# Optimization experiments

Hardware: AMD Instinct MI355X
Metric: run time of the kernel (lower is better)

The kernel has to match this reference:

```python
import jax, jax.numpy as jnp
import numpy as np

B, N, E = 16, 5000, 40000
IN_DIM, HID, GRU_OUT = 128, 512, 16
G0, G1, G2 = 1, 128, 128          # gcn_dim = [1,128,128]
M0, M1, M2 = 512, 1024, N * GRU_OUT  # gru_out_linear MLP dims (hidden_num prepended)
EPS = 1e-5                         # BatchNorm1d eps (eval: running mean 0, var 1)


def _gcn_norm(edge_index, n):
    loop = jnp.arange(n)
    src = jnp.concatenate([edge_index[0], loop])
    dst = jnp.concatenate([edge_index[1], loop])
    deg = jax.ops.segment_sum(jnp.ones(src.shape[0], jnp.float32), dst, num_segments=n)
    dinv = 1.0 / jnp.sqrt(deg)
    return src, dst, dinv[src] * dinv[dst]


def _gcn_conv(h, W, b, src, dst, norm):
    hw = jnp.einsum('bnf,fg->bng', h, W)
    msgs = hw[:, src, :] * norm[None, :, None]            # [B,E+N,Fout]
    agg = jax.ops.segment_sum(jnp.swapaxes(msgs, 0, 1), dst, num_segments=h.shape[1])
    return jnp.swapaxes(agg, 0, 1) + b


def _gru_cell(x, h, Wih, Whh, bih, bhh):
    gi = x @ Wih.T + bih
    gh = h @ Whh.T + bhh
    ir, iz, ig = jnp.split(gi, 3, axis=-1)
    hr, hz, hg = jnp.split(gh, 3, axis=-1)
    r = jax.nn.sigmoid(ir + hr)
    z = jax.nn.sigmoid(iz + hz)
    n = jnp.tanh(ig + r * hg)
    return (1.0 - z) * n + z * h


def _mlp_block(x, W, b, a, g, be):
    # Dropout(eval)=Identity -> Linear -> PReLU -> BatchNorm1d(eval, rm=0, rv=1)
    y = x @ W.T + b
    y = jnp.where(y >= 0, y, a * y)
    return y / jnp.sqrt(1.0 + EPS) * g + be


def setup_inputs():
    key = jax.random.key(0)
    ks = jax.random.split(key, 32)
    f = lambda i, shp, s=0.02: jax.random.normal(ks[i], shp, jnp.float32) * s
    return dict(
        x=jax.random.normal(ks[0], (B, IN_DIM), jnp.float32),
        smoothed_vert_pos=jax.random.normal(ks[1], (B, N * 3), jnp.float32),
        edge_index=jax.random.randint(ks[2], (2, E), 0, N),
        Wih=f(3, (3 * HID, IN_DIM)), Whh=f(4, (3 * HID, HID)),
        bih=f(5, (3 * HID,)), bhh=f(6, (3 * HID,)),
        Wg1=f(7, (G0, G1), 0.1), bg1=f(8, (G1,)),
        Wg2=f(9, (G1, G2), 0.1), bg2=f(10, (G2,)),
        W1=f(11, (M1, M0)), b1=f(12, (M1,)),
        a1=jnp.full((M1,), 0.25, jnp.float32),
        g1=1.0 + f(13, (M1,)), be1=f(14, (M1,)),
        W2=f(15, (M2, M1), 0.01), b2=f(16, (M2,)),
        a2=jnp.full((M2,), 0.25, jnp.float32),
        g2=1.0 + f(17, (M2,)), be2=f(18, (M2,)),
        Wo=f(19, (1, G2 + GRU_OUT)), bo=f(20, (1,)),
    )


def reference(x, smoothed_vert_pos, edge_index, Wih, Whh, bih, bhh,
              Wg1, bg1, Wg2, bg2, W1, b1, a1, g1, be1,
              W2, b2, a2, g2, be2, Wo, bo):
    b = x.shape[0]
    svp = smoothed_vert_pos.reshape(b, N, 3)
    src, dst, norm = _gcn_norm(edge_index, N)
    z = svp[:, :, 2:3]                                   # channel j+2, j=0
    h1 = _gcn_conv(z, Wg1, bg1, src, dst, norm)          # [B,N,G1], no nonlinearity between convs (as in source)
    res = _gcn_conv(h1, Wg2, bg2, src, dst, norm)        # [B,N,G2]
    hidden = jnp.zeros((b, HID), x.dtype)                # hidden=None path
    next_hidden = _gru_cell(x, hidden, Wih, Whh, bih, bhh)
    m = _mlp_block(next_hidden, W1, b1, a1, g1, be1)
    m = _mlp_block(m, W2, b2, a2, g2, be2)
    gru_out = m.reshape(b, N, GRU_OUT)
    y = jnp.concatenate([gru_out, res], axis=2) @ Wo.T + bo  # [B,N,1]
    return y.reshape(b, N), next_hidden
```

## Files before the change

### kernel.cpp

```cpp
#include <hip/hip_runtime.h>
#include <hip/hip_bf16.h>

#define NN 5000
#define BB 16
#define EE 40000
#define INF 128
#define HID 512
#define M1D 1024
#define EPSV 1e-5f

typedef float f4 __attribute__((ext_vector_type(4)));

__device__ __forceinline__ float dot4(f4 a, f4 b) {
    return fmaf(a.x, b.x, fmaf(a.y, b.y, fmaf(a.z, b.z, a.w * b.w)));
}
__device__ __forceinline__ f4 ntload(const float* p) {
    return __builtin_nontemporal_load((const f4*)p);
}

#define GRU_BLOCKS 128
#define DEG_BLOCKS 157
#define ZPACK_BLOCKS 313
#define ZERO_BLOCKS 157

__global__ __launch_bounds__(256)
void k_s1(const int* __restrict__ ei, const float* __restrict__ x,
          const float* __restrict__ svp,
          const float* __restrict__ Wih, const float* __restrict__ bih,
          const float* __restrict__ bhh,
          const float* __restrict__ Wg1, const float* __restrict__ bg1,
          const float* __restrict__ Wg2, const float* __restrict__ bg2,
          const float* __restrict__ Wo, const float* __restrict__ bo,
          float* __restrict__ deg, float* __restrict__ nh,
          float* __restrict__ outNH, float* __restrict__ cst,
          float* __restrict__ zpack, float* __restrict__ zerobase) {
    const int blk = blockIdx.x;
    const int tid = threadIdx.x;

    if (blk < GRU_BLOCKS) {
        const int t = blk * 256 + tid;
        const int q = t & 3, idx = t >> 2;
        const int b = idx >> 9, h = idx & 511;
        const float* xb = x + b * INF;
        const float* wr = Wih + (size_t)h * INF;
        const float* wz = Wih + (size_t)(HID + h) * INF;
        const float* wg = Wih + (size_t)(2 * HID + h) * INF;
        float ir = 0.f, iz = 0.f, ig = 0.f;
        #pragma unroll 8
        for (int i = 0; i < 8; ++i) {
            const int k0 = i * 16 + q * 4;
            const f4 xv = *(const f4*)(xb + k0);
            ir += dot4(xv, *(const f4*)(wr + k0));
            iz += dot4(xv, *(const f4*)(wz + k0));
            ig += dot4(xv, *(const f4*)(wg + k0));
        }
        ir += __shfl_xor(ir, 1); ir += __shfl_xor(ir, 2);
        iz += __shfl_xor(iz, 1); iz += __shfl_xor(iz, 2);
        ig += __shfl_xor(ig, 1); ig += __shfl_xor(ig, 2);
        if (q == 0) {
            ir += bih[h]; iz += bih[HID + h]; ig += bih[2 * HID + h];
            float r  = 1.f / (1.f + expf(-(ir + bhh[h])));
            float z  = 1.f / (1.f + expf(-(iz + bhh[HID + h])));
            float nv = tanhf(ig + r * bhh[2 * HID + h]);
            float v  = (1.f - z) * nv;
            nh[idx] = v;
            outNH[idx] = v;
        }
    } else if (blk < GRU_BLOCKS + DEG_BLOCKS) {
        const int e = (blk - GRU_BLOCKS) * 256 + tid;
        if (e < EE) atomicAdd(&deg[ei[EE + e]], 1.0f);
    } else if (blk == GRU_BLOCKS + DEG_BLOCKS) {
        __shared__ float su[128], sv[128], sc[128];
        const int g = tid;
        if (g < 128) {
            float t = 0.f;
            for (int c = 0; c < 128; ++c) t = fmaf(Wg2[g * 128 + c], Wo[16 + c], t);
            su[g] = Wg1[g] * t;
            sv[g] = bg1[g] * t;
            sc[g] = bg2[g] * Wo[16 + g];
        }
        __syncthreads();
        for (int s = 64; s > 0; s >>= 1) {
            if (g < s) { su[g] += su[g + s]; sv[g] += sv[g + s]; sc[g] += sc[g + s]; }
            __syncthreads();
        }
        if (g == 0) { cst[0] = su[0]; cst[1] = sv[0]; cst[2] = sc[0] + bo[0]; }
    } else if (blk < GRU_BLOCKS + DEG_BLOCKS + 1 + ZPACK_BLOCKS) {
        const int t = (blk - (GRU_BLOCKS + DEG_BLOCKS + 1)) * 256 + tid;
        if (t < NN * BB) {
            const int n = t >> 4, b = t & 15;
            zpack[t] = svp[b * (NN * 3) + 3 * n + 2];
        }
    } else {
        const int t = (blk - (GRU_BLOCKS + DEG_BLOCKS + 1 + ZPACK_BLOCKS)) * 256 + tid;
        if (t < 2 * BB * NN / 4) ((f4*)zerobase)[t] = (f4)(0.f);
    }
}

#define AGG1_BLOCKS 2500
#define MLP_BLOCKS 256

__global__ __launch_bounds__(256)
void k_s2(const int* __restrict__ ei, const float* __restrict__ deg,
          const float* __restrict__ zpack, const float* __restrict__ nh,
          const float* __restrict__ W1, const float* __restrict__ b1,
          const float* __restrict__ a1, const float* __restrict__ g1,
          const float* __restrict__ be1,
          float* __restrict__ m1, float* __restrict__ aggzE, float* __restrict__ s1E) {
    const int blk = blockIdx.x;
    const int tid = threadIdx.x;

    if (blk < AGG1_BLOCKS) {
        const int t = blk * 256 + tid;
        const int e = t >> 4, b = t & 15;
        const int s = ei[e], d = ei[EE + e];
        const float w = rsqrtf(1.f + deg[s]) * rsqrtf(1.f + deg[d]);
        atomicAdd(&aggzE[d * 16 + b], w * zpack[s * 16 + b]);
        if (b == 0) atomicAdd(&s1E[d], w);
    } else {
        const int t = (blk - AGG1_BLOCKS) * 256 + tid;
        const int q = t & 3, idx = t >> 2;
        const int b = idx >> 10, i = idx & 1023;
        const float* hb = nh + b * HID;
        const float* wr = W1 + (size_t)i * HID;
        float acc = 0.f;
        #pragma unroll 8
        for (int ii = 0; ii < 32; ++ii) {
            const int k0 = ii * 16 + q * 4;
            acc += dot4(*(const f4*)(hb + k0), *(const f4*)(wr + k0));
        }
        acc += __shfl_xor(acc, 1); acc += __shfl_xor(acc, 2);
        if (q == 0) {
            acc += b1[i];
            float v = acc >= 0.f ? acc : a1[i] * acc;
            m1[idx] = v * (1.f / sqrtf(1.f + EPSV)) * g1[i] + be1[i];
        }
    }
}

#define BIG_BLOCKS 1000
#define AGG2_BLOCKS 2500

__global__ __launch_bounds__(256, 4)
void k_s3(const float* __restrict__ W2, const float* __restrict__ m1,
          const float* __restrict__ b2, const float* __restrict__ a2,
          const float* __restrict__ g2, const float* __restrict__ be2,
          const float* __restrict__ Wo,
          const int* __restrict__ ei, const float* __restrict__ deg,
          const float* __restrict__ zpack, const float* __restrict__ aggzE,
          float* __restrict__ aggz2E, float* __restrict__ ysum) {
    __shared__ float accs[4][80][16];
    const int blk = blockIdx.x;
    const int tid = threadIdx.x;

    if (blk < BIG_BLOCKS) {
        const int w = tid >> 6, l = tid & 63;
        const int koff = w * 256 + l * 4;
        const int n0 = blk * 5;
        const int jbase = n0 * 16;

        float4 m1r[16];
        #pragma unroll
        for (int b = 0; b < 16; ++b)
            m1r[b] = *(const float4*)(m1 + b * M1D + koff);

        const int hi0 = l & 1, hi1 = (l >> 1) & 1, hi2 = (l >> 2) & 1, hi3 = (l >> 3) & 1;
        const int brev = ((l & 1) << 3) | ((l & 2) << 1) | ((l & 4) >> 1) | ((l & 8) >> 3);

        const float* wp = W2 + (size_t)jbase * M1D + koff;
        f4 w0 = ntload(wp);
        f4 w1 = ntload(wp + M1D);
        for (int jj = 0; jj < 80; ++jj) {
            const int jn = (jj + 2 < 80) ? (jj + 2) : 79;
            const f4 wn = ntload(wp + (size_t)jn * M1D);
            float acc[16];
            #pragma unroll
            for (int b = 0; b < 16; ++b)
                acc[b] = fmaf(w0.x, m1r[b].x, fmaf(w0.y, m1r[b].y,
                         fmaf(w0.z, m1r[b].z, w0.w * m1r[b].w)));
            float r8[8];
            #pragma unroll
            for (int i = 0; i < 8; ++i) {
                float keep = hi0 ? acc[8 + i] : acc[i];
                float send = hi0 ? acc[i]     : acc[8 + i];
                r8[i] = keep + __shfl_xor(send, 1, 64);
            }
            float r4[4];
            #pragma unroll
            for (int i = 0; i < 4; ++i) {
                float keep = hi1 ? r8[4 + i] : r8[i];
                float send = hi1 ? r8[i]     : r8[4 + i];
                r4[i] = keep + __shfl_xor(send, 2, 64);
            }
            float r2[2];
            #pragma unroll
            for (int i = 0; i < 2; ++i) {
                float keep = hi2 ? r4[2 + i] : r4[i];
                float send = hi2 ? r4[i]     : r4[2 + i];
                r2[i] = keep + __shfl_xor(send, 4, 64);
            }
            float keep = hi3 ? r2[1] : r2[0];
            float send = hi3 ? r2[0] : r2[1];
            float r1 = keep + __shfl_xor(send, 8, 64);
            r1 += __shfl_xor(r1, 16, 64);
            r1 += __shfl_xor(r1, 32, 64);
            if (l < 16) accs[w][jj][brev] = r1;
            w0 = w1; w1 = wn;
        }
        __syncthreads();

        if (tid < 80) {
            const int nl = tid >> 4, b = tid & 15;
            const float invs = 1.f / sqrtf(1.f + EPSV);
            float sum = 0.f;
            #pragma unroll
            for (int kk = 0; kk < 16; ++kk) {
                const int rloc = nl * 16 + kk;
                const int j = jbase + rloc;
                float a = accs[0][rloc][b] + accs[1][rloc][b]
                        + accs[2][rloc][b] + accs[3][rloc][b] + b2[j];
                float v = a >= 0.f ? a : a2[j] * a;
                float val = v * invs * g2[j] + be2[j];
                sum = fmaf(val, Wo[kk], sum);
            }
            ysum[n0 * 16 + tid] = sum;
        }
    } else {
        const int t = (blk - BIG_BLOCKS) * 256 + tid;
        const int e = t >> 4, b = t & 15;
        const int s = ei[e], d = ei[EE + e];
        const float degs = deg[s];
        const float d2s = 1.f / (1.f + degs);
        const float w = rsqrtf(1.f + degs) * rsqrtf(1.f + deg[d]);
        const float A1s = aggzE[s * 16 + b] + d2s * zpack[s * 16 + b];
        atomicAdd(&aggz2E[d * 16 + b], w * A1s);
    }
}

__global__ __launch_bounds__(256)
void k_fin(const float* __restrict__ ysum, const float* __restrict__ aggzE,
           const float* __restrict__ aggz2E, const float* __restrict__ s1E,
           const float* __restrict__ deg, const float* __restrict__ zpack,
           const float* __restrict__ cst, float* __restrict__ y) {
    const int t = blockIdx.x * 256 + threadIdx.x;
    if (t >= BB * NN) return;
    const int b = t / NN, n = t % NN;
    const float U = cst[0], V = cst[1], C0 = cst[2];
    const float d2 = 1.f / (1.f + deg[n]);
    const float z  = zpack[n * 16 + b];
    const float A1 = aggzE[n * 16 + b] + d2 * z;
    const float A2 = aggz2E[n * 16 + b] + d2 * A1;
    const float S1v = s1E[n] + d2;
    y[t] = ysum[n * 16 + b] + U * A2 + V * S1v + C0;
}


extern "C" void kernel_launch(void* const* d_in, const int* in_sizes, int n_in,
                              void* d_out, int out_size, void* d_ws, size_t ws_size,
                              hipStream_t stream) {
    const float* x   = (const float*)d_in[0];
    const float* svp = (const float*)d_in[1];
    const int*   ei  = (const int*)d_in[2];
    const float* Wih = (const float*)d_in[3];
    const float* bih = (const float*)d_in[5];
    const float* bhh = (const float*)d_in[6];
    const float* Wg1 = (const float*)d_in[7];
    const float* bg1 = (const float*)d_in[8];
    const float* Wg2 = (const float*)d_in[9];
    const float* bg2 = (const float*)d_in[10];
    const float* W1  = (const float*)d_in[11];
    const float* b1  = (const float*)d_in[12];
    const float* a1  = (const float*)d_in[13];
    const float* g1  = (const float*)d_in[14];
    const float* be1 = (const float*)d_in[15];
    const float* W2  = (const float*)d_in[16];
    const float* b2  = (const float*)d_in[17];
    const float* a2  = (const float*)d_in[18];
    const float* g2  = (const float*)d_in[19];
    const float* be2 = (const float*)d_in[20];
    const float* Wo  = (const float*)d_in[21];
    const float* bo  = (const float*)d_in[22];
    float* out = (float*)d_out;

    float* ws      = (float*)d_ws;
    float* deg     = ws;
    float* s1E     = deg + NN;
    float* aggzE   = s1E + NN;
    float* aggz2E  = aggzE + BB * NN;
    float* zpack   = aggz2E + BB * NN;
    float* ysum    = zpack + BB * NN;
    float* nh      = ysum + BB * NN;
    float* m1      = nh + BB * HID;
    float* cst     = m1 + BB * M1D;

    hipMemsetAsync(ws, 0, (size_t)(2 * NN) * sizeof(float), stream);

    k_s1<<<dim3(GRU_BLOCKS + DEG_BLOCKS + 1 + ZPACK_BLOCKS + ZERO_BLOCKS),
           dim3(256), 0, stream>>>(
        ei, x, svp, Wih, bih, bhh, Wg1, bg1, Wg2, bg2, Wo, bo,
        deg, nh, out + BB * NN, cst, zpack, aggzE );

    k_s2<<<dim3(AGG1_BLOCKS + MLP_BLOCKS), dim3(256), 0, stream>>>(
        ei, deg, zpack, nh, W1, b1, a1, g1, be1, m1, aggzE, s1E);

    k_s3<<<dim3(BIG_BLOCKS + AGG2_BLOCKS), dim3(256), 0, stream>>>(
        W2, m1, b2, a2, g2, be2, Wo, ei, deg, zpack, aggzE, aggz2E, ysum);

    k_fin<<<dim3((BB * NN + 255) / 256), dim3(256), 0, stream>>>(
        ysum, aggzE, aggz2E, s1E, deg, zpack, cst, out);
}
```

Before: 117.6 us.

## Split W2 GEMV into halves overlapped with each GCN aggregation pass

Restructures the launch schedule. The 80K-row W2 GEMV is split into two 500-block halves, each co-scheduled with one of the two edge-aggregation passes, so the atomic-heavy scatter work overlaps the bandwidth-bound weight stream. The memset is replaced by a zeroing pre-kernel, and the first-layer MLP becomes its own small kernel. Cross-lane reductions in the GEMV now use DPP moves instead of shuffles, and the final kernel reads node-major buffers contiguously. The cost is one more kernel launch and a serialised MLP step.

New measurement: 139.8 us. +18.9%, slower.

```diff
diff --git a/kernel.cpp b/kernel.cpp
--- a/kernel.cpp
+++ b/kernel.cpp
@@ -17,26 +17,66 @@
 __device__ __forceinline__ f4 ntload(const float* p) {
     return __builtin_nontemporal_load((const f4*)p);
 }
+__device__ __forceinline__ float dpp_xor1(float x) {
+    return __int_as_float(__builtin_amdgcn_update_dpp(0, __float_as_int(x), 0xB1, 0xF, 0xF, true));
+}
+__device__ __forceinline__ float dpp_xor2(float x) {
+    return __int_as_float(__builtin_amdgcn_update_dpp(0, __float_as_int(x), 0x4E, 0xF, 0xF, true));
+}
+__device__ __forceinline__ float dpp_xor8(float x) {
+    return __int_as_float(__builtin_amdgcn_update_dpp(0, __float_as_int(x), 0x128, 0xF, 0xF, true));
+}
+
+#define ZERO_BLOCKS 167
+#define ZPACK_BLOCKS 313
+
+__global__ __launch_bounds__(256)
+void k_pre(const float* __restrict__ svp,
+           const float* __restrict__ Wg1, const float* __restrict__ bg1,
+           const float* __restrict__ Wg2, const float* __restrict__ bg2,
+           const float* __restrict__ Wo, const float* __restrict__ bo,
+           float* __restrict__ zerobase, float* __restrict__ zpack,
+           float* __restrict__ cst) {
+    const int blk = blockIdx.x;
+    const int tid = threadIdx.x;
+    if (blk < ZERO_BLOCKS) {
+        const int t = blk * 256 + tid;
+        if (t < (2 * NN + 2 * BB * NN) / 4) ((f4*)zerobase)[t] = (f4)(0.f);
+    } else if (blk < ZERO_BLOCKS + ZPACK_BLOCKS) {
+        const int t = (blk - ZERO_BLOCKS) * 256 + tid;
+        if (t < NN * BB) {
+            const int n = t >> 4, b = t & 15;
+            zpack[t] = svp[b * (NN * 3) + 3 * n + 2];
+        }
+    } else {
+        __shared__ float su[128], sv[128], sc[128];
+        const int g = tid;
+        if (g < 128) {
+            float t = 0.f;
+            for (int c = 0; c < 128; ++c) t = fmaf(Wg2[g * 128 + c], Wo[16 + c], t);
+            su[g] = Wg1[g] * t;
+            sv[g] = bg1[g] * t;
+            sc[g] = bg2[g] * Wo[16 + g];
+        }
+        __syncthreads();
+        for (int s = 64; s > 0; s >>= 1) {
+            if (g < s) { su[g] += su[g + s]; sv[g] += sv[g + s]; sc[g] += sc[g + s]; }
+            __syncthreads();
+        }
+        if (g == 0) { cst[0] = su[0]; cst[1] = sv[0]; cst[2] = sc[0] + bo[0]; }
+    }
+}
 
 #define GRU_BLOCKS 128
 #define DEG_BLOCKS 157
-#define ZPACK_BLOCKS 313
-#define ZERO_BLOCKS 157
 
 __global__ __launch_bounds__(256)
-void k_s1(const int* __restrict__ ei, const float* __restrict__ x,
-          const float* __restrict__ svp,
+void k_gd(const int* __restrict__ ei, const float* __restrict__ x,
           const float* __restrict__ Wih, const float* __restrict__ bih,
           const float* __restrict__ bhh,
-          const float* __restrict__ Wg1, const float* __restrict__ bg1,
-          const float* __restrict__ Wg2, const float* __restrict__ bg2,
-          const float* __restrict__ Wo, const float* __restrict__ bo,
-          float* __restrict__ deg, float* __restrict__ nh,
-          float* __restrict__ outNH, float* __restrict__ cst,
-          float* __restrict__ zpack, float* __restrict__ zerobase) {
+          float* __restrict__ deg, float* __restrict__ nh, float* __restrict__ outNH) {
     const int blk = blockIdx.x;
     const int tid = threadIdx.x;
-
     if (blk < GRU_BLOCKS) {
         const int t = blk * 256 + tid;
         const int q = t & 3, idx = t >> 2;
@@ -66,97 +106,56 @@
             nh[idx] = v;
             outNH[idx] = v;
         }
-    } else if (blk < GRU_BLOCKS + DEG_BLOCKS) {
+    } else {
         const int e = (blk - GRU_BLOCKS) * 256 + tid;
         if (e < EE) atomicAdd(&deg[ei[EE + e]], 1.0f);
-    } else if (blk == GRU_BLOCKS + DEG_BLOCKS) {
-        __shared__ float su[128], sv[128], sc[128];
-        const int g = tid;
-        if (g < 128) {
-            float t = 0.f;
-            for (int c = 0; c < 128; ++c) t = fmaf(Wg2[g * 128 + c], Wo[16 + c], t);
-            su[g] = Wg1[g] * t;
-            sv[g] = bg1[g] * t;
-            sc[g] = bg2[g] * Wo[16 + g];
-        }
-        __syncthreads();
-        for (int s = 64; s > 0; s >>= 1) {
-            if (g < s) { su[g] += su[g + s]; sv[g] += sv[g + s]; sc[g] += sc[g + s]; }
-            __syncthreads();
-        }
-        if (g == 0) { cst[0] = su[0]; cst[1] = sv[0]; cst[2] = sc[0] + bo[0]; }
-    } else if (blk < GRU_BLOCKS + DEG_BLOCKS + 1 + ZPACK_BLOCKS) {
-        const int t = (blk - (GRU_BLOCKS + DEG_BLOCKS + 1)) * 256 + tid;
-        if (t < NN * BB) {
-            const int n = t >> 4, b = t & 15;
-            zpack[t] = svp[b * (NN * 3) + 3 * n + 2];
-        }
-    } else {
-        const int t = (blk - (GRU_BLOCKS + DEG_BLOCKS + 1 + ZPACK_BLOCKS)) * 256 + tid;
-        if (t < 2 * BB * NN / 4) ((f4*)zerobase)[t] = (f4)(0.f);
-    }
-}
-
-#define AGG1_BLOCKS 2500
-#define MLP_BLOCKS 256
+    }
+}
 
 __global__ __launch_bounds__(256)
-void k_s2(const int* __restrict__ ei, const float* __restrict__ deg,
-          const float* __restrict__ zpack, const float* __restrict__ nh,
-          const float* __restrict__ W1, const float* __restrict__ b1,
-          const float* __restrict__ a1, const float* __restrict__ g1,
-          const float* __restrict__ be1,
-          float* __restrict__ m1, float* __restrict__ aggzE, float* __restrict__ s1E) {
-    const int blk = blockIdx.x;
-    const int tid = threadIdx.x;
-
-    if (blk < AGG1_BLOCKS) {
-        const int t = blk * 256 + tid;
-        const int e = t >> 4, b = t & 15;
-        const int s = ei[e], d = ei[EE + e];
-        const float w = rsqrtf(1.f + deg[s]) * rsqrtf(1.f + deg[d]);
-        atomicAdd(&aggzE[d * 16 + b], w * zpack[s * 16 + b]);
-        if (b == 0) atomicAdd(&s1E[d], w);
-    } else {
-        const int t = (blk - AGG1_BLOCKS) * 256 + tid;
-        const int q = t & 3, idx = t >> 2;
-        const int b = idx >> 10, i = idx & 1023;
-        const float* hb = nh + b * HID;
-        const float* wr = W1 + (size_t)i * HID;
-        float acc = 0.f;
-        #pragma unroll 8
-        for (int ii = 0; ii < 32; ++ii) {
-            const int k0 = ii * 16 + q * 4;
-            acc += dot4(*(const f4*)(hb + k0), *(const f4*)(wr + k0));
-        }
-        acc += __shfl_xor(acc, 1); acc += __shfl_xor(acc, 2);
-        if (q == 0) {
-            acc += b1[i];
-            float v = acc >= 0.f ? acc : a1[i] * acc;
-            m1[idx] = v * (1.f / sqrtf(1.f + EPSV)) * g1[i] + be1[i];
-        }
-    }
-}
-
-#define BIG_BLOCKS 1000
-#define AGG2_BLOCKS 2500
+void k_mlp(const float* __restrict__ nh,
+           const float* __restrict__ W1, const float* __restrict__ b1,
+           const float* __restrict__ a1, const float* __restrict__ g1,
+           const float* __restrict__ be1, float* __restrict__ m1) {
+    const int t = blockIdx.x * 256 + threadIdx.x;
+    const int q = t & 3, idx = t >> 2;
+    const int b = idx >> 10, i = idx & 1023;
+    const float* hb = nh + b * HID;
+    const float* wr = W1 + (size_t)i * HID;
+    float acc = 0.f;
+    #pragma unroll 8
+    for (int ii = 0; ii < 32; ++ii) {
+        const int k0 = ii * 16 + q * 4;
+        acc += dot4(*(const f4*)(hb + k0), *(const f4*)(wr + k0));
+    }
+    acc += __shfl_xor(acc, 1); acc += __shfl_xor(acc, 2);
+    if (q == 0) {
+        acc += b1[i];
+        float v = acc >= 0.f ? acc : a1[i] * acc;
+        m1[idx] = v * (1.f / sqrtf(1.f + EPSV)) * g1[i] + be1[i];
+    }
+}
+
+#define BIGH_BLOCKS 500
+#define AGG_BLOCKS 2500
 
 __global__ __launch_bounds__(256, 4)
-void k_s3(const float* __restrict__ W2, const float* __restrict__ m1,
-          const float* __restrict__ b2, const float* __restrict__ a2,
-          const float* __restrict__ g2, const float* __restrict__ be2,
-          const float* __restrict__ Wo,
-          const int* __restrict__ ei, const float* __restrict__ deg,
-          const float* __restrict__ zpack, const float* __restrict__ aggzE,
-          float* __restrict__ aggz2E, float* __restrict__ ysum) {
+void k_sAB(const float* __restrict__ W2, const float* __restrict__ m1,
+           const float* __restrict__ b2, const float* __restrict__ a2,
+           const float* __restrict__ g2, const float* __restrict__ be2,
+           const float* __restrict__ Wo,
+           const int* __restrict__ ei, const float* __restrict__ deg,
+           const float* __restrict__ zpack, float* __restrict__ aggzE,
+           float* __restrict__ aggz2E, float* __restrict__ s1E,
+           float* __restrict__ ysum, int nodeOff, int mode) {
     __shared__ float accs[4][80][16];
     const int blk = blockIdx.x;
     const int tid = threadIdx.x;
 
-    if (blk < BIG_BLOCKS) {
+    if (blk < BIGH_BLOCKS) {
         const int w = tid >> 6, l = tid & 63;
         const int koff = w * 256 + l * 4;
-        const int n0 = blk * 5;
+        const int n0 = nodeOff + blk * 5;
         const int jbase = n0 * 16;
 
         float4 m1r[16];
@@ -183,14 +182,14 @@
             for (int i = 0; i < 8; ++i) {
                 float keep = hi0 ? acc[8 + i] : acc[i];
                 float send = hi0 ? acc[i]     : acc[8 + i];
-                r8[i] = keep + __shfl_xor(send, 1, 64);
+                r8[i] = keep + dpp_xor1(send);
             }
             float r4[4];
             #pragma unroll
             for (int i = 0; i < 4; ++i) {
                 float keep = hi1 ? r8[4 + i] : r8[i];
                 float send = hi1 ? r8[i]     : r8[4 + i];
-                r4[i] = keep + __shfl_xor(send, 2, 64);
+                r4[i] = keep + dpp_xor2(send);
             }
             float r2[2];
             #pragma unroll
@@ -201,7 +200,7 @@
             }
             float keep = hi3 ? r2[1] : r2[0];
             float send = hi3 ? r2[0] : r2[1];
-            float r1 = keep + __shfl_xor(send, 8, 64);
+            float r1 = keep + dpp_xor8(send);
             r1 += __shfl_xor(r1, 16, 64);
             r1 += __shfl_xor(r1, 32, 64);
             if (l < 16) accs[w][jj][brev] = r1;
@@ -226,14 +225,19 @@
             ysum[n0 * 16 + tid] = sum;
         }
     } else {
-        const int t = (blk - BIG_BLOCKS) * 256 + tid;
+        const int t = (blk - BIGH_BLOCKS) * 256 + tid;
         const int e = t >> 4, b = t & 15;
         const int s = ei[e], d = ei[EE + e];
         const float degs = deg[s];
-        const float d2s = 1.f / (1.f + degs);
         const float w = rsqrtf(1.f + degs) * rsqrtf(1.f + deg[d]);
-        const float A1s = aggzE[s * 16 + b] + d2s * zpack[s * 16 + b];
-        atomicAdd(&aggz2E[d * 16 + b], w * A1s);
+        if (mode == 0) {
+            atomicAdd(&aggzE[d * 16 + b], w * zpack[s * 16 + b]);
+            if (b == 0) atomicAdd(&s1E[d], w);
+        } else {
+            const float d2s = 1.f / (1.f + degs);
+            const float A1s = aggzE[s * 16 + b] + d2s * zpack[s * 16 + b];
+            atomicAdd(&aggz2E[d * 16 + b], w * A1s);
+        }
     }
 }
 
@@ -244,14 +248,14 @@
            const float* __restrict__ cst, float* __restrict__ y) {
     const int t = blockIdx.x * 256 + threadIdx.x;
     if (t >= BB * NN) return;
-    const int b = t / NN, n = t % NN;
+    const int n = t >> 4, b = t & 15;
     const float U = cst[0], V = cst[1], C0 = cst[2];
     const float d2 = 1.f / (1.f + deg[n]);
-    const float z  = zpack[n * 16 + b];
-    const float A1 = aggzE[n * 16 + b] + d2 * z;
-    const float A2 = aggz2E[n * 16 + b] + d2 * A1;
+    const float z  = zpack[t];
+    const float A1 = aggzE[t] + d2 * z;
+    const float A2 = aggz2E[t] + d2 * A1;
     const float S1v = s1E[n] + d2;
-    y[t] = ysum[n * 16 + b] + U * A2 + V * S1v + C0;
+    y[b * NN + n] = ysum[t] + U * A2 + V * S1v + C0;
 }
 
 
@@ -293,18 +297,22 @@
     float* m1      = nh + BB * HID;
     float* cst     = m1 + BB * M1D;
 
-    hipMemsetAsync(ws, 0, (size_t)(2 * NN) * sizeof(float), stream);
-
-    k_s1<<<dim3(GRU_BLOCKS + DEG_BLOCKS + 1 + ZPACK_BLOCKS + ZERO_BLOCKS),
-           dim3(256), 0, stream>>>(
-        ei, x, svp, Wih, bih, bhh, Wg1, bg1, Wg2, bg2, Wo, bo,
-        deg, nh, out + BB * NN, cst, zpack, aggzE );
-
-    k_s2<<<dim3(AGG1_BLOCKS + MLP_BLOCKS), dim3(256), 0, stream>>>(
-        ei, deg, zpack, nh, W1, b1, a1, g1, be1, m1, aggzE, s1E);
-
-    k_s3<<<dim3(BIG_BLOCKS + AGG2_BLOCKS), dim3(256), 0, stream>>>(
-        W2, m1, b2, a2, g2, be2, Wo, ei, deg, zpack, aggzE, aggz2E, ysum);
+    k_pre<<<dim3(ZERO_BLOCKS + ZPACK_BLOCKS + 1), dim3(256), 0, stream>>>(
+        svp, Wg1, bg1, Wg2, bg2, Wo, bo, deg , zpack, cst);
+
+    k_gd<<<dim3(GRU_BLOCKS + DEG_BLOCKS), dim3(256), 0, stream>>>(
+        ei, x, Wih, bih, bhh, deg, nh, out + BB * NN);
+
+    k_mlp<<<dim3(256), dim3(256), 0, stream>>>(
+        nh, W1, b1, a1, g1, be1, m1);
+
+    k_sAB<<<dim3(BIGH_BLOCKS + AGG_BLOCKS), dim3(256), 0, stream>>>(
+        W2, m1, b2, a2, g2, be2, Wo, ei, deg, zpack, aggzE, aggz2E, s1E, ysum,
+        0, 0);
+
+    k_sAB<<<dim3(BIGH_BLOCKS + AGG_BLOCKS), dim3(256), 0, stream>>>(
+        W2, m1, b2, a2, g2, be2, Wo, ei, deg, zpack, aggzE, aggz2E, s1E, ysum,
+        2500, 1);
 
     k_fin<<<dim3((BB * NN + 255) / 256), dim3(256), 0, stream>>>(
         ysum, aggzE, aggz2E, s1E, deg, zpack, cst, out);
```
